# Kernel tuning notes

Hardware: AMD Instinct MI355X
Metric: run time of the kernel (lower is better)

## Reference

```python
import jax, jax.numpy as jnp
import numpy as np

M, N, D, H, E = 100000, 50000, 128, 2, 1000000
NEG_SLOPE = 0.2  # standard GAT LeakyReLU slope


def setup_inputs() -> dict:
    key = jax.random.key(0)
    ks = jax.random.split(key, 14)
    inp = {
        "u_prev": jax.random.normal(ks[0], (M, D), jnp.float32),
        "i_prev": jax.random.normal(ks[1], (N, D), jnp.float32),
        "w_user": jax.random.normal(ks[2], (D, D), jnp.float32) * 0.05,
        "b_user": jax.random.normal(ks[3], (D,), jnp.float32) * 0.05,
        "w_item": jax.random.normal(ks[4], (D, D), jnp.float32) * 0.05,
        "b_item": jax.random.normal(ks[5], (D,), jnp.float32) * 0.05,
        "a_u_src": jax.random.normal(ks[6], (H, D), jnp.float32) * 0.1,
        "a_u_dst": jax.random.normal(ks[7], (H, D), jnp.float32) * 0.1,
        "a_i_src": jax.random.normal(ks[8], (H, D), jnp.float32) * 0.1,
        "a_i_dst": jax.random.normal(ks[9], (H, D), jnp.float32) * 0.1,
        "u2i_row": jax.random.randint(ks[10], (E,), 0, M, jnp.int32),
        "u2i_col": jax.random.randint(ks[11], (E,), 0, N, jnp.int32),
        "i2u_row": jax.random.randint(ks[12], (E,), 0, N, jnp.int32),
        "i2u_col": jax.random.randint(ks[13], (E,), 0, M, jnp.int32),
    }
    return inp


def _segment_softmax(logits, seg, num_segments):
    # neighborhood softmax: normalize per adjacency row
    mx = jax.ops.segment_max(logits, seg, num_segments=num_segments)
    e = jnp.exp(logits - mx[seg])
    s = jax.ops.segment_sum(e, seg, num_segments=num_segments)
    return e / s[seg]


def _attend(row, col, h_src, h_dst, a_src, a_dst, num_src):
    hs = h_src[row]  # (E, D) gather of source-node features
    hd = h_dst[col]  # (E, D) gather of dest-node features
    head_outs = []
    for h in range(a_src.shape[0]):  # small fixed head count
        logits = jax.nn.leaky_relu(hs @ a_src[h] + hd @ a_dst[h], NEG_SLOPE)  # (E,)
        att = _segment_softmax(logits, row, num_src)                         # (E,)
        # sparse att @ h_dst == row-segment sum of att-weighted neighbor features
        head_outs.append(jax.ops.segment_sum(att[:, None] * hd, row, num_segments=num_src))
    out = sum(head_outs) / len(head_outs)  # reduce_att = mean over heads
    return jax.nn.elu(out)                  # self.nonlinear


def reference(u_prev, i_prev, w_user, b_user, w_item, b_item,
              a_u_src, a_u_dst, a_i_src, a_i_dst,
              u2i_row, u2i_col, i2u_row, i2u_col):
    u = u_prev @ w_user + b_user  # (M, D)
    i = i_prev @ w_item + b_item  # (N, D)
    u_next = _attend(u2i_row, u2i_col, u, i, a_u_src, a_u_dst, M)
    i_next = _attend(i2u_row, i2u_col, i, u, a_i_src, a_i_dst, N)
    return (u_next, i_next)
```

## Files before the change

kernel.cpp:

```cpp
#include <hip/hip_runtime.h>
#include <cstdint>
#include <cstddef>

#define D 128
#define NEG_SLOPE 0.2f

__device__ __forceinline__ float lrelu(float x) { return x > 0.0f ? x : NEG_SLOPE * x; }
__device__ __forceinline__ float elu_f(float x) { return x > 0.0f ? x : expm1f(x); }
__device__ __forceinline__ unsigned short f2bf(float f) {
    unsigned u = __float_as_uint(f);
    return (unsigned short)((u + 0x7fffu + ((u >> 16) & 1u)) >> 16);
}

struct GemmDir {
    const float* A; const float* W; const float* bias;
    const float* v0; const float* v1; const float* v2; const float* v3;
    unsigned short* Cb;
    float4* att; int R;
};

__global__ __launch_bounds__(256) void gemm_att_hist(
    GemmDir g0, int nb0, GemmDir g1, int nbG,
    const int* __restrict__ rowA, int* __restrict__ cntA, int EA,
    const int* __restrict__ rowB, int* __restrict__ cntB, int EB, int histHalf)
{
    int nbHist = 2 * histHalf;
    if ((int)blockIdx.x < nbHist) {
        bool dB = (int)blockIdx.x >= histHalf;
        const int* row = dB ? rowB : rowA;
        int* cnt = dB ? cntB : cntA;
        int E = dB ? EB : EA;
        int i = (dB ? blockIdx.x - histHalf : blockIdx.x) * 256 + threadIdx.x;
        int stride = histHalf * 256;
        for (; i < E; i += stride) atomicAdd(&cnt[row[i]], 1);
        return;
    }
    int gb = blockIdx.x - nbHist;
    const bool second = gb >= nb0;
    GemmDir g = second ? g1 : g0;
    const int bid = second ? (gb - nb0) : gb;
    (void)nbG;

    __shared__ float As[64][33];
    __shared__ float Ws[32][128];
    const int tid = threadIdx.x;
    const int row0 = bid * 64;
    const int cr = tid & 15;
    const int rr = tid >> 4;

    float acc[4][8];
#pragma unroll
    for (int i = 0; i < 4; ++i)
#pragma unroll
        for (int j = 0; j < 8; ++j) acc[i][j] = 0.0f;

    for (int kc = 0; kc < 128; kc += 32) {
#pragma unroll
        for (int q = 0; q < 2; ++q) {
            int f = tid * 2 + q;
            int r = f >> 3, kq = f & 7;
            int gr = row0 + r; if (gr > g.R - 1) gr = g.R - 1;
            const float4 a = *(const float4*)(g.A + (size_t)gr * D + kc + kq * 4);
            As[r][kq * 4 + 0] = a.x; As[r][kq * 4 + 1] = a.y;
            As[r][kq * 4 + 2] = a.z; As[r][kq * 4 + 3] = a.w;
        }
#pragma unroll
        for (int q = 0; q < 4; ++q) {
            int f = tid + q * 256;
            int k = f >> 5, c4 = f & 31;
            *(float4*)&Ws[k][c4 * 4] = *(const float4*)(g.W + (size_t)(kc + k) * D + c4 * 4);
        }
        __syncthreads();
#pragma unroll
        for (int k = 0; k < 32; ++k) {
            float a0 = As[rr * 4 + 0][k];
            float a1 = As[rr * 4 + 1][k];
            float a2 = As[rr * 4 + 2][k];
            float a3 = As[rr * 4 + 3][k];
            float4 w0 = *(const float4*)&Ws[k][cr * 4];
            float4 w1 = *(const float4*)&Ws[k][64 + cr * 4];
            acc[0][0] += a0 * w0.x; acc[0][1] += a0 * w0.y; acc[0][2] += a0 * w0.z; acc[0][3] += a0 * w0.w;
            acc[0][4] += a0 * w1.x; acc[0][5] += a0 * w1.y; acc[0][6] += a0 * w1.z; acc[0][7] += a0 * w1.w;
            acc[1][0] += a1 * w0.x; acc[1][1] += a1 * w0.y; acc[1][2] += a1 * w0.z; acc[1][3] += a1 * w0.w;
            acc[1][4] += a1 * w1.x; acc[1][5] += a1 * w1.y; acc[1][6] += a1 * w1.z; acc[1][7] += a1 * w1.w;
            acc[2][0] += a2 * w0.x; acc[2][1] += a2 * w0.y; acc[2][2] += a2 * w0.z; acc[2][3] += a2 * w0.w;
            acc[2][4] += a2 * w1.x; acc[2][5] += a2 * w1.y; acc[2][6] += a2 * w1.z; acc[2][7] += a2 * w1.w;
            acc[3][0] += a3 * w0.x; acc[3][1] += a3 * w0.y; acc[3][2] += a3 * w0.z; acc[3][3] += a3 * w0.w;
            acc[3][4] += a3 * w1.x; acc[3][5] += a3 * w1.y; acc[3][6] += a3 * w1.z; acc[3][7] += a3 * w1.w;
        }
        __syncthreads();
    }

    float4 b0 = *(const float4*)(g.bias + cr * 4);
    float4 b1 = *(const float4*)(g.bias + 64 + cr * 4);
#pragma unroll
    for (int i = 0; i < 4; ++i) {
        acc[i][0] += b0.x; acc[i][1] += b0.y; acc[i][2] += b0.z; acc[i][3] += b0.w;
        acc[i][4] += b1.x; acc[i][5] += b1.y; acc[i][6] += b1.z; acc[i][7] += b1.w;
    }
#pragma unroll
    for (int i = 0; i < 4; ++i) {
        int row = row0 + rr * 4 + i;
        if (row < g.R) {
            ushort4 s0 = { f2bf(acc[i][0]), f2bf(acc[i][1]), f2bf(acc[i][2]), f2bf(acc[i][3]) };
            ushort4 s1 = { f2bf(acc[i][4]), f2bf(acc[i][5]), f2bf(acc[i][6]), f2bf(acc[i][7]) };
            *(ushort4*)(g.Cb + (size_t)row * D + cr * 4) = s0;
            *(ushort4*)(g.Cb + (size_t)row * D + 64 + cr * 4) = s1;
        }
    }

    const float* vs[4] = { g.v0, g.v1, g.v2, g.v3 };
    float p[4][4];
#pragma unroll
    for (int h = 0; h < 4; ++h) {
        float4 va = *(const float4*)(vs[h] + cr * 4);
        float4 vb = *(const float4*)(vs[h] + 64 + cr * 4);
#pragma unroll
        for (int i = 0; i < 4; ++i) {
            p[i][h] = acc[i][0] * va.x + acc[i][1] * va.y + acc[i][2] * va.z + acc[i][3] * va.w
                    + acc[i][4] * vb.x + acc[i][5] * vb.y + acc[i][6] * vb.z + acc[i][7] * vb.w;
        }
    }
#pragma unroll
    for (int i = 0; i < 4; ++i)
#pragma unroll
        for (int h = 0; h < 4; ++h)
#pragma unroll
            for (int o = 1; o < 16; o <<= 1)
                p[i][h] += __shfl_xor(p[i][h], o, 64);
    if (cr == 0) {
#pragma unroll
        for (int i = 0; i < 4; ++i) {
            int row = row0 + rr * 4 + i;
            if (row < g.R) g.att[row] = make_float4(p[i][0], p[i][1], p[i][2], p[i][3]);
        }
    }
}

__device__ __forceinline__ void scan1_body(const int* counts, int* offsets, int* blockSums,
                                           int S, int bid)
{
    __shared__ int s[256];
    int tid = threadIdx.x;
    int i = bid * 256 + tid;
    int v = (i < S) ? counts[i] : 0;
    s[tid] = v;
    __syncthreads();
    for (int o = 1; o < 256; o <<= 1) {
        int t = (tid >= o) ? s[tid - o] : 0;
        __syncthreads();
        s[tid] += t;
        __syncthreads();
    }
    if (i < S) offsets[i + 1] = s[tid];
    if (tid == 255) blockSums[bid] = s[255];
}

__global__ __launch_bounds__(256) void scan1_both(const int* cA, int* offA, int* bsA, int SA, int nbA,
                                                  const int* cB, int* offB, int* bsB, int SB)
{
    if (blockIdx.x < (unsigned)nbA) scan1_body(cA, offA, bsA, SA, blockIdx.x);
    else scan1_body(cB, offB, bsB, SB, blockIdx.x - nbA);
}

__global__ __launch_bounds__(512) void scan2_both(int* sumsA, int nbA, int* sumsB, int nbB)
{
    int* sums = blockIdx.x ? sumsB : sumsA;
    int nb = blockIdx.x ? nbB : nbA;
    __shared__ int s[512];
    int tid = threadIdx.x;
    int v = (tid < nb) ? sums[tid] : 0;
    s[tid] = v;
    __syncthreads();
    for (int o = 1; o < 512; o <<= 1) {
        int t = (tid >= o) ? s[tid - o] : 0;
        __syncthreads();
        s[tid] += t;
        __syncthreads();
    }
    if (tid < nb) sums[tid] = s[tid] - v;
}

__device__ __forceinline__ void scan3_body(const int* counts, int* offsets, int* cursor,
                                           const int* blockSums, int S, int bid)
{
    int i = bid * 256 + threadIdx.x;
    if (i >= S) return;
    int incl = offsets[i + 1] + blockSums[bid];
    offsets[i + 1] = incl;
    cursor[i] = incl - counts[i];
    if (i == 0) offsets[0] = 0;
}

__global__ __launch_bounds__(256) void scan3_both(const int* cA, int* offA, int* curA, const int* bsA, int SA, int nbA,
                                                  const int* cB, int* offB, int* curB, const int* bsB, int SB)
{
    if (blockIdx.x < (unsigned)nbA) scan3_body(cA, offA, curA, bsA, SA, blockIdx.x);
    else scan3_body(cB, offB, curB, bsB, SB, blockIdx.x - nbA);
}

__global__ __launch_bounds__(256) void scatter_both(
    const int* __restrict__ rowA, const int* __restrict__ colA,
    int* __restrict__ curA, int* __restrict__ scolA, int EA, int chunkA,
    const int* __restrict__ rowB, const int* __restrict__ colB,
    int* __restrict__ curB, int* __restrict__ scolB, int EB, int chunkB)
{
    int half = gridDim.x >> 1;
    bool dB = (int)blockIdx.x >= half;
    int b = dB ? (int)blockIdx.x - half : (int)blockIdx.x;
    const int* row = dB ? rowB : rowA;
    const int* col = dB ? colB : colA;
    int* cursor = dB ? curB : curA;
    int* scol = dB ? scolB : scolA;
    int E = dB ? EB : EA;
    int chunk = dB ? chunkB : chunkA;

    int part = b & 7;
    int idx  = b >> 3;
    int nper = half >> 3;
    int lo = part * chunk, hi = lo + chunk;

    for (int i = idx * 256 + (int)threadIdx.x; i < E; i += nper * 256) {
        int r = row[i];
        if (r >= lo && r < hi) {
            int pos = atomicAdd(&cursor[r], 1);
            scol[pos] = col[i];
        }
    }
}

__device__ __forceinline__ void aggregate_row(
    const int* __restrict__ offsets, const int* __restrict__ scol,
    const char* __restrict__ satt, const char* __restrict__ datt,
    const unsigned short* __restrict__ featb,
    float* __restrict__ out, int seg, int lane)
{
    int beg = offsets[seg], end = offsets[seg + 1];
    int deg = end - beg;
    float2 sa = *(const float2*)(satt + (size_t)seg * 16);
    float accx = 0.0f, accy = 0.0f;
    if (deg > 0 && deg <= 64) {
        int myc = 0;
        float e0 = 0.0f, e1 = 0.0f;
        if (lane < deg) {
            myc = scol[beg + lane];
            float2 da = *(const float2*)(datt + (size_t)myc * 16);
            e0 = __expf(lrelu(sa.x + da.x));
            e1 = __expf(lrelu(sa.y + da.y));
        }
        float s0 = e0, s1 = e1;
#pragma unroll
        for (int o = 32; o > 0; o >>= 1) {
            s0 += __shfl_xor(s0, o, 64);
            s1 += __shfl_xor(s1, o, 64);
        }
        float myw = e0 * (0.5f / s0) + e1 * (0.5f / s1);
        float a0x = 0.f, a0y = 0.f, a1x = 0.f, a1y = 0.f,
              a2x = 0.f, a2y = 0.f, a3x = 0.f, a3y = 0.f;
        int j = 0;
        for (; j + 4 <= deg; j += 4) {
            int c0 = __shfl(myc, j, 64), c1 = __shfl(myc, j + 1, 64);
            int c2 = __shfl(myc, j + 2, 64), c3 = __shfl(myc, j + 3, 64);
            float w0 = __shfl(myw, j, 64), w1 = __shfl(myw, j + 1, 64);
            float w2 = __shfl(myw, j + 2, 64), w3 = __shfl(myw, j + 3, 64);
            unsigned f0 = *(const unsigned*)(featb + (size_t)c0 * D + 2 * lane);
            unsigned f1 = *(const unsigned*)(featb + (size_t)c1 * D + 2 * lane);
            unsigned f2 = *(const unsigned*)(featb + (size_t)c2 * D + 2 * lane);
            unsigned f3 = *(const unsigned*)(featb + (size_t)c3 * D + 2 * lane);
            a0x += w0 * __uint_as_float(f0 << 16); a0y += w0 * __uint_as_float(f0 & 0xffff0000u);
            a1x += w1 * __uint_as_float(f1 << 16); a1y += w1 * __uint_as_float(f1 & 0xffff0000u);
            a2x += w2 * __uint_as_float(f2 << 16); a2y += w2 * __uint_as_float(f2 & 0xffff0000u);
            a3x += w3 * __uint_as_float(f3 << 16); a3y += w3 * __uint_as_float(f3 & 0xffff0000u);
        }
        for (; j < deg; ++j) {
            int c0 = __shfl(myc, j, 64);
            float w0 = __shfl(myw, j, 64);
            unsigned f0 = *(const unsigned*)(featb + (size_t)c0 * D + 2 * lane);
            a0x += w0 * __uint_as_float(f0 << 16); a0y += w0 * __uint_as_float(f0 & 0xffff0000u);
        }
        accx = (a0x + a1x) + (a2x + a3x);
        accy = (a0y + a1y) + (a2y + a3y);
    } else if (deg > 64) {
        float s0 = 0.0f, s1 = 0.0f;
        for (int p = beg + lane; p < end; p += 64) {
            int c = scol[p];
            float2 da = *(const float2*)(datt + (size_t)c * 16);
            s0 += __expf(lrelu(sa.x + da.x));
            s1 += __expf(lrelu(sa.y + da.y));
        }
#pragma unroll
        for (int o = 32; o > 0; o >>= 1) {
            s0 += __shfl_xor(s0, o, 64);
            s1 += __shfl_xor(s1, o, 64);
        }
        float inv0 = 0.5f / s0, inv1 = 0.5f / s1;
        for (int p = beg; p < end; ++p) {
            int c = scol[p];
            float2 da = *(const float2*)(datt + (size_t)c * 16);
            float w = __expf(lrelu(sa.x + da.x)) * inv0 + __expf(lrelu(sa.y + da.y)) * inv1;
            unsigned f = *(const unsigned*)(featb + (size_t)c * D + 2 * lane);
            accx += w * __uint_as_float(f << 16);
            accy += w * __uint_as_float(f & 0xffff0000u);
        }
    }
    *(float2*)(out + (size_t)seg * D + 2 * lane) = make_float2(elu_f(accx), elu_f(accy));
}

__global__ __launch_bounds__(256) void aggregate_both(
    const int* offA, const int* scolA, const char* sattA, const char* dattA,
    const unsigned short* featA, float* outA, int SA, int nbA,
    const int* offB, const int* scolB, const char* sattB, const char* dattB,
    const unsigned short* featB, float* outB, int SB)
{
    int lane = threadIdx.x & 63;
    if (blockIdx.x < (unsigned)nbA) {
        int seg = blockIdx.x * 4 + (threadIdx.x >> 6);
        if (seg < SA) aggregate_row(offA, scolA, sattA, dattA, featA, outA, seg, lane);
    } else {
        int seg = (blockIdx.x - nbA) * 4 + (threadIdx.x >> 6);
        if (seg < SB) aggregate_row(offB, scolB, sattB, dattB, featB, outB, seg, lane);
    }
}

extern "C" void kernel_launch(void* const* d_in, const int* in_sizes, int n_in,
                              void* d_out, int out_size, void* d_ws, size_t ws_size,
                              hipStream_t stream)
{
    const float* u_prev  = (const float*)d_in[0];
    const float* i_prev  = (const float*)d_in[1];
    const float* w_user  = (const float*)d_in[2];
    const float* b_user  = (const float*)d_in[3];
    const float* w_item  = (const float*)d_in[4];
    const float* b_item  = (const float*)d_in[5];
    const float* a_u_src = (const float*)d_in[6];
    const float* a_u_dst = (const float*)d_in[7];
    const float* a_i_src = (const float*)d_in[8];
    const float* a_i_dst = (const float*)d_in[9];
    const int* u2i_row = (const int*)d_in[10];
    const int* u2i_col = (const int*)d_in[11];
    const int* i2u_row = (const int*)d_in[12];
    const int* i2u_col = (const int*)d_in[13];

    const int M = in_sizes[0] / D;
    const int N = in_sizes[1] / D;
    const int EA = in_sizes[10];
    const int EB = in_sizes[12];

    char* ws = (char*)d_ws;
    size_t off = 0;
    auto carve = [&](size_t bytes) -> char* {
        char* p = ws + off;
        off += (bytes + 255) & ~(size_t)255;
        return p;
    };
    unsigned short* u_featb = (unsigned short*)carve((size_t)M * D * 2);
    unsigned short* i_featb = (unsigned short*)carve((size_t)N * D * 2);
    float4* u_att    = (float4*)carve((size_t)M * 16);
    float4* i_att    = (float4*)carve((size_t)N * 16);
    int*    countsA  = (int*)carve((size_t)M * 4);
    int*    offsetsA = (int*)carve((size_t)(M + 1) * 4);
    int*    cursorA  = (int*)carve((size_t)M * 4);
    int*    bsumsA   = (int*)carve(512 * 4);
    int*    scolA    = (int*)carve((size_t)EA * 4);
    int*    countsB  = (int*)carve((size_t)N * 4);
    int*    offsetsB = (int*)carve((size_t)(N + 1) * 4);
    int*    cursorB  = (int*)carve((size_t)N * 4);
    int*    bsumsB   = (int*)carve(512 * 4);
    int*    scolB    = (int*)carve((size_t)EB * 4);
    (void)ws_size; (void)n_in; (void)out_size;

    hipMemsetAsync(countsA, 0, (size_t)M * 4, stream);
    hipMemsetAsync(countsB, 0, (size_t)N * 4, stream);

    GemmDir gu = { u_prev, w_user, b_user, a_u_src, a_u_src + D, a_i_dst, a_i_dst + D, u_featb, u_att, M };
    GemmDir gi = { i_prev, w_item, b_item, a_u_dst, a_u_dst + D, a_i_src, a_i_src + D, i_featb, i_att, N };
    int nbGu = (M + 63) / 64, nbGi = (N + 63) / 64;
    int histHalf = 512;
    gemm_att_hist<<<2 * histHalf + nbGu + nbGi, 256, 0, stream>>>(
        gu, nbGu, gi, nbGu + nbGi,
        u2i_row, countsA, EA, i2u_row, countsB, EB, histHalf);

    int nbA = (M + 255) / 256, nbB = (N + 255) / 256;
    scan1_both<<<nbA + nbB, 256, 0, stream>>>(countsA, offsetsA, bsumsA, M, nbA,
                                              countsB, offsetsB, bsumsB, N);
    scan2_both<<<2, 512, 0, stream>>>(bsumsA, nbA, bsumsB, nbB);
    scan3_both<<<nbA + nbB, 256, 0, stream>>>(countsA, offsetsA, cursorA, bsumsA, M, nbA,
                                              countsB, offsetsB, cursorB, bsumsB, N);

    int chunkA = (M + 7) / 8, chunkB = (N + 7) / 8;
    scatter_both<<<2048, 256, 0, stream>>>(u2i_row, u2i_col, cursorA, scolA, EA, chunkA,
                                           i2u_row, i2u_col, cursorB, scolB, EB, chunkB);

    float* out_u = (float*)d_out;
    float* out_i = out_u + (size_t)M * D;
    int nbAggA = (M + 3) / 4, nbAggB = (N + 3) / 4;
    aggregate_both<<<nbAggA + nbAggB, 256, 0, stream>>>(
        offsetsA, scolA, (const char*)u_att, (const char*)i_att, i_featb, out_u, M, nbAggA,
        offsetsB, scolB, (const char*)i_att + 8, (const char*)u_att + 8, u_featb, out_i, N);
}
```

Baseline: 473.9 us.

## Replace FP32 FMA projection GEMM with bf16 MFMA and swizzled LDS weights

New measurement: 499.3 us. 5.4% more time.

```diff
diff --git a/kernel.cpp b/kernel.cpp
--- a/kernel.cpp
+++ b/kernel.cpp
@@ -11,6 +11,9 @@
     unsigned u = __float_as_uint(f);
     return (unsigned short)((u + 0x7fffu + ((u >> 16) & 1u)) >> 16);
 }
+
+typedef __attribute__((ext_vector_type(8))) short bf16x8;
+typedef __attribute__((ext_vector_type(4))) float f32x4;
 
 struct GemmDir {
     const float* A; const float* W; const float* bias;
@@ -41,71 +44,72 @@
     const int bid = second ? (gb - nb0) : gb;
     (void)nbG;
 
-    __shared__ float As[64][33];
-    __shared__ float Ws[32][128];
+    __shared__ unsigned short Wl[128 * 128];
+
     const int tid = threadIdx.x;
     const int row0 = bid * 64;
-    const int cr = tid & 15;
-    const int rr = tid >> 4;
-
-    float acc[4][8];
-#pragma unroll
-    for (int i = 0; i < 4; ++i)
-#pragma unroll
-        for (int j = 0; j < 8; ++j) acc[i][j] = 0.0f;
-
-    for (int kc = 0; kc < 128; kc += 32) {
-#pragma unroll
-        for (int q = 0; q < 2; ++q) {
-            int f = tid * 2 + q;
-            int r = f >> 3, kq = f & 7;
-            int gr = row0 + r; if (gr > g.R - 1) gr = g.R - 1;
-            const float4 a = *(const float4*)(g.A + (size_t)gr * D + kc + kq * 4);
-            As[r][kq * 4 + 0] = a.x; As[r][kq * 4 + 1] = a.y;
-            As[r][kq * 4 + 2] = a.z; As[r][kq * 4 + 3] = a.w;
-        }
-#pragma unroll
-        for (int q = 0; q < 4; ++q) {
-            int f = tid + q * 256;
-            int k = f >> 5, c4 = f & 31;
-            *(float4*)&Ws[k][c4 * 4] = *(const float4*)(g.W + (size_t)(kc + k) * D + c4 * 4);
-        }
-        __syncthreads();
-#pragma unroll
-        for (int k = 0; k < 32; ++k) {
-            float a0 = As[rr * 4 + 0][k];
-            float a1 = As[rr * 4 + 1][k];
-            float a2 = As[rr * 4 + 2][k];
-            float a3 = As[rr * 4 + 3][k];
-            float4 w0 = *(const float4*)&Ws[k][cr * 4];
-            float4 w1 = *(const float4*)&Ws[k][64 + cr * 4];
-            acc[0][0] += a0 * w0.x; acc[0][1] += a0 * w0.y; acc[0][2] += a0 * w0.z; acc[0][3] += a0 * w0.w;
-            acc[0][4] += a0 * w1.x; acc[0][5] += a0 * w1.y; acc[0][6] += a0 * w1.z; acc[0][7] += a0 * w1.w;
-            acc[1][0] += a1 * w0.x; acc[1][1] += a1 * w0.y; acc[1][2] += a1 * w0.z; acc[1][3] += a1 * w0.w;
-            acc[1][4] += a1 * w1.x; acc[1][5] += a1 * w1.y; acc[1][6] += a1 * w1.z; acc[1][7] += a1 * w1.w;
-            acc[2][0] += a2 * w0.x; acc[2][1] += a2 * w0.y; acc[2][2] += a2 * w0.z; acc[2][3] += a2 * w0.w;
-            acc[2][4] += a2 * w1.x; acc[2][5] += a2 * w1.y; acc[2][6] += a2 * w1.z; acc[2][7] += a2 * w1.w;
-            acc[3][0] += a3 * w0.x; acc[3][1] += a3 * w0.y; acc[3][2] += a3 * w0.z; acc[3][3] += a3 * w0.w;
-            acc[3][4] += a3 * w1.x; acc[3][5] += a3 * w1.y; acc[3][6] += a3 * w1.z; acc[3][7] += a3 * w1.w;
-        }
-        __syncthreads();
-    }
-
-    float4 b0 = *(const float4*)(g.bias + cr * 4);
-    float4 b1 = *(const float4*)(g.bias + 64 + cr * 4);
-#pragma unroll
-    for (int i = 0; i < 4; ++i) {
-        acc[i][0] += b0.x; acc[i][1] += b0.y; acc[i][2] += b0.z; acc[i][3] += b0.w;
-        acc[i][4] += b1.x; acc[i][5] += b1.y; acc[i][6] += b1.z; acc[i][7] += b1.w;
-    }
-#pragma unroll
-    for (int i = 0; i < 4; ++i) {
-        int row = row0 + rr * 4 + i;
+    const int wave = tid >> 6;
+    const int lane = tid & 63;
+    const int lm = lane & 15;
+    const int lg = lane >> 4;
+
+#pragma unroll
+    for (int q = 0; q < 8; ++q) {
+        int c = tid + q * 256;
+        int n = c >> 4;
+        int s = c & 15;
+        const float* src = g.W + (size_t)(s * 8) * D + n;
+        unsigned t0 = ((unsigned)f2bf(src[0 * D])) | ((unsigned)f2bf(src[1 * D]) << 16);
+        unsigned t1 = ((unsigned)f2bf(src[2 * D])) | ((unsigned)f2bf(src[3 * D]) << 16);
+        unsigned t2 = ((unsigned)f2bf(src[4 * D])) | ((unsigned)f2bf(src[5 * D]) << 16);
+        unsigned t3 = ((unsigned)f2bf(src[6 * D])) | ((unsigned)f2bf(src[7 * D]) << 16);
+        uint4 pk = make_uint4(t0, t1, t2, t3);
+        *(uint4*)((char*)Wl + n * 256 + ((s * 16) ^ ((n & 7) << 4))) = pk;
+    }
+    __syncthreads();
+
+    int ar = row0 + (wave << 4) + lm;
+    if (ar > g.R - 1) ar = g.R - 1;
+    const float* Arow = g.A + (size_t)ar * D;
+
+    f32x4 acc[8];
+#pragma unroll
+    for (int nt = 0; nt < 8; ++nt) { acc[nt][0] = 0.f; acc[nt][1] = 0.f; acc[nt][2] = 0.f; acc[nt][3] = 0.f; }
+
+    const int xr = (lm & 7) << 4;
+#pragma unroll
+    for (int ks = 0; ks < 4; ++ks) {
+        const float4 a0 = *(const float4*)(Arow + ks * 32 + lg * 8);
+        const float4 a1 = *(const float4*)(Arow + ks * 32 + lg * 8 + 4);
+        bf16x8 af;
+        af[0] = (short)f2bf(a0.x); af[1] = (short)f2bf(a0.y);
+        af[2] = (short)f2bf(a0.z); af[3] = (short)f2bf(a0.w);
+        af[4] = (short)f2bf(a1.x); af[5] = (short)f2bf(a1.y);
+        af[6] = (short)f2bf(a1.z); af[7] = (short)f2bf(a1.w);
+        const int slot = ks * 4 + lg;
+        const char* bbase = (const char*)Wl + lm * 256 + ((slot * 16) ^ xr);
+#pragma unroll
+        for (int nt = 0; nt < 8; ++nt) {
+            bf16x8 bf = *(const bf16x8*)(bbase + nt * 4096);
+            acc[nt] = __builtin_amdgcn_mfma_f32_16x16x32_bf16(af, bf, acc[nt], 0, 0, 0);
+        }
+    }
+
+    float bcol[8];
+#pragma unroll
+    for (int nt = 0; nt < 8; ++nt) bcol[nt] = g.bias[nt * 16 + lm];
+#pragma unroll
+    for (int nt = 0; nt < 8; ++nt)
+#pragma unroll
+        for (int r = 0; r < 4; ++r) acc[nt][r] += bcol[nt];
+
+#pragma unroll
+    for (int r = 0; r < 4; ++r) {
+        int row = row0 + (wave << 4) + (lg << 2) + r;
         if (row < g.R) {
-            ushort4 s0 = { f2bf(acc[i][0]), f2bf(acc[i][1]), f2bf(acc[i][2]), f2bf(acc[i][3]) };
-            ushort4 s1 = { f2bf(acc[i][4]), f2bf(acc[i][5]), f2bf(acc[i][6]), f2bf(acc[i][7]) };
-            *(ushort4*)(g.Cb + (size_t)row * D + cr * 4) = s0;
-            *(ushort4*)(g.Cb + (size_t)row * D + 64 + cr * 4) = s1;
+#pragma unroll
+            for (int nt = 0; nt < 8; ++nt)
+                g.Cb[(size_t)row * D + nt * 16 + lm] = f2bf(acc[nt][r]);
         }
     }
 
@@ -113,26 +117,29 @@
     float p[4][4];
 #pragma unroll
     for (int h = 0; h < 4; ++h) {
-        float4 va = *(const float4*)(vs[h] + cr * 4);
-        float4 vb = *(const float4*)(vs[h] + 64 + cr * 4);
-#pragma unroll
-        for (int i = 0; i < 4; ++i) {
-            p[i][h] = acc[i][0] * va.x + acc[i][1] * va.y + acc[i][2] * va.z + acc[i][3] * va.w
-                    + acc[i][4] * vb.x + acc[i][5] * vb.y + acc[i][6] * vb.z + acc[i][7] * vb.w;
-        }
-    }
-#pragma unroll
-    for (int i = 0; i < 4; ++i)
+        float vv[8];
+#pragma unroll
+        for (int nt = 0; nt < 8; ++nt) vv[nt] = vs[h][nt * 16 + lm];
+#pragma unroll
+        for (int r = 0; r < 4; ++r) {
+            float s = 0.f;
+#pragma unroll
+            for (int nt = 0; nt < 8; ++nt) s += acc[nt][r] * vv[nt];
+            p[r][h] = s;
+        }
+    }
+#pragma unroll
+    for (int r = 0; r < 4; ++r)
 #pragma unroll
         for (int h = 0; h < 4; ++h)
 #pragma unroll
             for (int o = 1; o < 16; o <<= 1)
-                p[i][h] += __shfl_xor(p[i][h], o, 64);
-    if (cr == 0) {
-#pragma unroll
-        for (int i = 0; i < 4; ++i) {
-            int row = row0 + rr * 4 + i;
-            if (row < g.R) g.att[row] = make_float4(p[i][0], p[i][1], p[i][2], p[i][3]);
+                p[r][h] += __shfl_xor(p[r][h], o, 64);
+    if (lm == 0) {
+#pragma unroll
+        for (int r = 0; r < 4; ++r) {
+            int row = row0 + (wave << 4) + (lg << 2) + r;
+            if (row < g.R) g.att[row] = make_float4(p[r][0], p[r][1], p[r][2], p[r][3]);
         }
     }
 }
```
